# Kernel tuning notes

Hardware: AMD Instinct MI355X
Metric: run time of the kernel (lower is better)

## Reference

```python
import jax, jax.numpy as jnp
import numpy as np

NEG_SLOPE = 0.2  # PyG GATConv default leaky_relu slope


def gat_conv(x, src, dst, num_nodes, W, att_src, att_dst, bias, heads, out_ch, concat):
    """PyG-style GATConv (eval mode, self-loops already included in src/dst).
    x: [N, in_ch]; src/dst: [E] int; W: [in_ch, heads*out_ch];
    att_src/att_dst: [heads, out_ch]; bias: [heads*out_ch] or [out_ch].
    """
    N = num_nodes
    h = (x @ W).reshape(N, heads, out_ch)                      # [N, H, C]
    a_src = jnp.einsum('nhc,hc->nh', h, att_src)               # [N, H]
    a_dst = jnp.einsum('nhc,hc->nh', h, att_dst)               # [N, H]
    e = jax.nn.leaky_relu(a_src[src] + a_dst[dst], NEG_SLOPE)  # [E, H]
    # segment softmax over incoming edges of each dst node
    m = jax.ops.segment_max(e, dst, num_segments=N)            # [N, H]
    m = jnp.where(jnp.isfinite(m), m, 0.0)
    w = jnp.exp(e - m[dst])                                    # [E, H]
    denom = jax.ops.segment_sum(w, dst, num_segments=N)        # [N, H]
    alpha = w / denom[dst]                                     # [E, H]
    msg = alpha[:, :, None] * h[src]                           # [E, H, C]
    out = jax.ops.segment_sum(msg, dst, num_segments=N)        # [N, H, C]
    if concat:
        out = out.reshape(N, heads * out_ch)
    else:
        out = out.mean(axis=1)
    return out + bias


def setup_inputs() -> dict:
    key = jax.random.key(0)
    ks = jax.random.split(key, 10)
    N, E, in_ch, hidden, heads = 50000, 800000, 128, 64, 4
    x = jax.random.normal(ks[0], (N, in_ch), dtype=jnp.float32)
    edge_index = jax.random.randint(ks[1], (2, E), 0, N, dtype=jnp.int64)
    s1 = float(np.sqrt(1.0 / in_ch))
    W1 = jax.random.normal(ks[2], (in_ch, heads * hidden), dtype=jnp.float32) * s1
    att_src1 = jax.random.normal(ks[3], (heads, hidden), dtype=jnp.float32) * 0.1
    att_dst1 = jax.random.normal(ks[4], (heads, hidden), dtype=jnp.float32) * 0.1
    bias1 = jnp.zeros((heads * hidden,), dtype=jnp.float32)
    s2 = float(np.sqrt(1.0 / (heads * hidden)))
    W2 = jax.random.normal(ks[5], (heads * hidden, 1), dtype=jnp.float32) * s2
    att_src2 = jax.random.normal(ks[6], (1, 1), dtype=jnp.float32) * 0.1
    att_dst2 = jax.random.normal(ks[7], (1, 1), dtype=jnp.float32) * 0.1
    bias2 = jnp.zeros((1,), dtype=jnp.float32)
    return {"x": x, "edge_index": edge_index, "W1": W1, "att_src1": att_src1,
            "att_dst1": att_dst1, "bias1": bias1, "W2": W2, "att_src2": att_src2,
            "att_dst2": att_dst2, "bias2": bias2}


def reference(x, edge_index, W1, att_src1, att_dst1, bias1, W2, att_src2, att_dst2, bias2):
    N = x.shape[0]
    hidden, heads = 64, 4
    loops = jnp.arange(N, dtype=edge_index.dtype)
    src = jnp.concatenate([edge_index[0], loops])  # PyG adds self-loops
    dst = jnp.concatenate([edge_index[1], loops])
    # eval mode -> dropout is identity
    h = gat_conv(x, src, dst, N, W1, att_src1, att_dst1, bias1, heads, hidden, True)
    h = jax.nn.elu(h)
    out = gat_conv(h, src, dst, N, W2, att_src2, att_dst2, bias2, 1, 1, False)
    return out.squeeze(-1)  # [N]
```

## Files before the change

kernel.cpp:

```cpp
#include <hip/hip_runtime.h>
#include <hip/hip_fp16.h>
#include <math.h>

#define INC 128
#define F1 256
#define HEADS 4
#define NEG_SLOPE 0.2f

typedef _Float16 f16x8 __attribute__((ext_vector_type(8)));
typedef float f32x4 __attribute__((ext_vector_type(4)));

__global__ __launch_bounds__(256) void prep_kernel(
    const float* __restrict__ W1, _Float16* __restrict__ W1T,
    const int* __restrict__ ei, int* __restrict__ deg, int* __restrict__ rank,
    int E, int Etot, int nw1t)
{
    int b = blockIdx.x;
    if (b < nw1t) {
        int i = b * 256 + threadIdx.x;
        int k = i >> 8;
        int c = i & 255;
        W1T[c * 128 + k] = (_Float16)W1[i];
    } else {
        int e = (b - nw1t) * 256 + threadIdx.x;
        if (e < Etot) {
            int d = (e < E) ? ei[E + e] : (e - E);
            rank[e] = atomicAdd(&deg[d], 1);
        }
    }
}

__global__ __launch_bounds__(256) void scan1_kernel(
    const int* __restrict__ deg, int* __restrict__ incl,
    int* __restrict__ bsum, int N)
{
    __shared__ int tmp[256];
    int i = blockIdx.x * 256 + threadIdx.x;
    int v = (i < N) ? deg[i] : 0;
    tmp[threadIdx.x] = v;
    __syncthreads();
    for (int o = 1; o < 256; o <<= 1) {
        int add = (threadIdx.x >= o) ? tmp[threadIdx.x - o] : 0;
        __syncthreads();
        tmp[threadIdx.x] += add;
        __syncthreads();
    }
    if (i < N) incl[i] = tmp[threadIdx.x];
    if (threadIdx.x == 255) bsum[blockIdx.x] = tmp[255];
}

__global__ __launch_bounds__(256) void scan3_kernel(
    const int* __restrict__ deg, const int* __restrict__ incl,
    const int* __restrict__ bsum, int* __restrict__ off,
    int N, int Etot, int nb)
{
    __shared__ int tmp[256];
    const int bid = blockIdx.x;
    const int t = threadIdx.x;
    tmp[t] = (t < bid && t < nb) ? bsum[t] : 0;
    __syncthreads();
    #pragma unroll
    for (int o = 128; o > 0; o >>= 1) {
        if (t < o) tmp[t] += tmp[t + o];
        __syncthreads();
    }
    int pre = tmp[0];
    int i = bid * 256 + t;
    if (i < N) {
        off[i] = incl[i] - deg[i] + pre;
    } else if (i == N) {
        off[N] = Etot;
    }
}

__global__ __launch_bounds__(256, 4) void gemm_fill_kernel(
    const float* __restrict__ x, const _Float16* __restrict__ W1T,
    const float* __restrict__ att_s, const float* __restrict__ att_d,
    __half* __restrict__ h1, float* __restrict__ a_src, float* __restrict__ a_dst,
    const int* __restrict__ ei, const int* __restrict__ rank,
    const int* __restrict__ off, int* __restrict__ esrc,
    int N, int E, int Etot, int ngemm)
{
    __shared__ __align__(16) char smem[64 * 264 * 2];

    if ((int)blockIdx.x >= ngemm) {
        int e = (blockIdx.x - ngemm) * 256 + threadIdx.x;
        if (e < Etot) {
            int s, d;
            if (e < E) { s = ei[e]; d = ei[E + e]; }
            else       { s = d = e - E; }
            esrc[off[d] + rank[e]] = s;
        }
        return;
    }

    _Float16* xh = (_Float16*)smem;
    _Float16* ol = (_Float16*)smem;

    const int tid = threadIdx.x;
    const int wave = tid >> 6;
    const int lane = tid & 63;
    const int q = lane >> 4;
    const int c16 = lane & 15;
    const int row0 = blockIdx.x * 64;

    #pragma unroll
    for (int it = 0; it < 8; ++it) {
        int idx = (tid + it * 256) << 2;
        int r = idx >> 7;
        int c = idx & 127;
        int row = row0 + r;
        float4 v = (row < N) ? *(const float4*)&x[(size_t)row * INC + c]
                             : make_float4(0.f, 0.f, 0.f, 0.f);
        __half2 p0 = __floats2half2_rn(v.x, v.y);
        __half2 p1 = __floats2half2_rn(v.z, v.w);
        uint2 pk;
        pk.x = *(unsigned int*)&p0;
        pk.y = *(unsigned int*)&p1;
        *(uint2*)&xh[r * 136 + c] = pk;
    }
    __syncthreads();

    f16x8 afrag[4];
    #pragma unroll
    for (int kc = 0; kc < 4; ++kc)
        afrag[kc] = *(const f16x8*)&xh[(wave * 16 + c16) * 136 + kc * 32 + q * 8];
    __syncthreads();

    float psS[4][4] = {};
    float psD[4][4] = {};

    #pragma unroll
    for (int nc = 0; nc < 16; ++nc) {
        const int head = nc >> 2;
        const int col = nc * 16 + c16;
        f32x4 acc = {0.f, 0.f, 0.f, 0.f};
        f16x8 b0 = *(const f16x8*)&W1T[(size_t)col * 128 + 0 * 32 + q * 8];
        f16x8 b1 = *(const f16x8*)&W1T[(size_t)col * 128 + 1 * 32 + q * 8];
        f16x8 b2 = *(const f16x8*)&W1T[(size_t)col * 128 + 2 * 32 + q * 8];
        f16x8 b3 = *(const f16x8*)&W1T[(size_t)col * 128 + 3 * 32 + q * 8];
        acc = __builtin_amdgcn_mfma_f32_16x16x32_f16(afrag[0], b0, acc, 0, 0, 0);
        acc = __builtin_amdgcn_mfma_f32_16x16x32_f16(afrag[1], b1, acc, 0, 0, 0);
        acc = __builtin_amdgcn_mfma_f32_16x16x32_f16(afrag[2], b2, acc, 0, 0, 0);
        acc = __builtin_amdgcn_mfma_f32_16x16x32_f16(afrag[3], b3, acc, 0, 0, 0);

        float avs = att_s[col];
        float avd = att_d[col];
        #pragma unroll
        for (int reg = 0; reg < 4; ++reg) {
            float v = acc[reg];
            psS[reg][head] += v * avs;
            psD[reg][head] += v * avd;
            int row = wave * 16 + q * 4 + reg;
            ol[row * 264 + col] = (_Float16)v;
        }
    }

    #pragma unroll
    for (int o = 1; o < 16; o <<= 1) {
        #pragma unroll
        for (int reg = 0; reg < 4; ++reg)
            #pragma unroll
            for (int h = 0; h < 4; ++h) {
                psS[reg][h] += __shfl_xor(psS[reg][h], o);
                psD[reg][h] += __shfl_xor(psD[reg][h], o);
            }
    }
    if (c16 == 0) {
        #pragma unroll
        for (int reg = 0; reg < 4; ++reg) {
            int row = row0 + wave * 16 + q * 4 + reg;
            if (row < N) {
                float4 vs = make_float4(psS[reg][0], psS[reg][1], psS[reg][2], psS[reg][3]);
                float4 vd = make_float4(psD[reg][0], psD[reg][1], psD[reg][2], psD[reg][3]);
                *(float4*)&a_src[row * HEADS] = vs;
                *(float4*)&a_dst[row * HEADS] = vd;
            }
        }
    }

    __syncthreads();
    {
        int r = tid >> 2;
        int cq = (tid & 3) * 64;
        int row = row0 + r;
        if (row < N) {
            #pragma unroll
            for (int j = 0; j < 8; ++j) {
                uint4 v = *(uint4*)&ol[r * 264 + cq + j * 8];
                *(uint4*)&h1[(size_t)row * F1 + cq + j * 8] = v;
            }
        }
    }
}

__global__ __launch_bounds__(256) void agg1_kernel(
    const __half* __restrict__ h1, const float* __restrict__ a_src,
    const float* __restrict__ a_dst, const int* __restrict__ off,
    const int* __restrict__ esrc, const float* __restrict__ bias1,
    const float* __restrict__ W2, float* __restrict__ z, int N)
{
    __shared__ unsigned lalh[4][64][4];
    __shared__ int lsrc_s[4][64];

    const int wave = threadIdx.x >> 6;
    const int lane = threadIdx.x & 63;
    const int n = blockIdx.x * 4 + wave;
    if (n >= N) return;

    const int beg = off[n], end = off[n + 1];
    const int deg = end - beg;
    const float4* a_src4 = (const float4*)a_src;
    const uint2* h2 = (const uint2*)h1;
    float4 ad4 = *(const float4*)&a_dst[n * HEADS];
    float ad[4] = {ad4.x, ad4.y, ad4.z, ad4.w};
    const int head = lane >> 4;

    __half2 acc01 = __float2half2_rn(0.f);
    __half2 acc23 = __float2half2_rn(0.f);

    #define GATHER(CNT)                                                          \
    {                                                                            \
        int j = 0;                                                               \
        for (; j + 4 <= (CNT); j += 4) {                                         \
            int s0 = lsrc_s[wave][j + 0];                                        \
            int s1 = lsrc_s[wave][j + 1];                                        \
            int s2 = lsrc_s[wave][j + 2];                                        \
            int s3 = lsrc_s[wave][j + 3];                                        \
            uint2 v0 = h2[(size_t)s0 * 64 + lane];                               \
            uint2 v1 = h2[(size_t)s1 * 64 + lane];                               \
            uint2 v2 = h2[(size_t)s2 * 64 + lane];                               \
            uint2 v3 = h2[(size_t)s3 * 64 + lane];                               \
            unsigned a0 = lalh[wave][j + 0][head];                               \
            unsigned a1 = lalh[wave][j + 1][head];                               \
            unsigned a2 = lalh[wave][j + 2][head];                               \
            unsigned a3 = lalh[wave][j + 3][head];                               \
            acc01 = __hfma2(*(__half2*)&a0, *(__half2*)&v0.x, acc01);            \
            acc23 = __hfma2(*(__half2*)&a0, *(__half2*)&v0.y, acc23);            \
            acc01 = __hfma2(*(__half2*)&a1, *(__half2*)&v1.x, acc01);            \
            acc23 = __hfma2(*(__half2*)&a1, *(__half2*)&v1.y, acc23);            \
            acc01 = __hfma2(*(__half2*)&a2, *(__half2*)&v2.x, acc01);            \
            acc23 = __hfma2(*(__half2*)&a2, *(__half2*)&v2.y, acc23);            \
            acc01 = __hfma2(*(__half2*)&a3, *(__half2*)&v3.x, acc01);            \
            acc23 = __hfma2(*(__half2*)&a3, *(__half2*)&v3.y, acc23);            \
        }                                                                        \
        for (; j < (CNT); ++j) {                                                 \
            int s0 = lsrc_s[wave][j];                                            \
            unsigned a0 = lalh[wave][j][head];                                   \
            uint2 v0 = h2[(size_t)s0 * 64 + lane];                               \
            acc01 = __hfma2(*(__half2*)&a0, *(__half2*)&v0.x, acc01);            \
            acc23 = __hfma2(*(__half2*)&a0, *(__half2*)&v0.y, acc23);            \
        }                                                                        \
    }

    if (deg <= 64) {
        int i = beg + lane;
        bool valid = i < end;
        int sN = esrc[valid ? i : beg];
        float4 a4 = a_src4[sN];
        float av[4] = {a4.x, a4.y, a4.z, a4.w};
        float ev[4];
        #pragma unroll
        for (int h = 0; h < 4; ++h) {
            float e = av[h] + ad[h];
            e = e > 0.f ? e : NEG_SLOPE * e;
            ev[h] = valid ? e : -1e30f;
        }
        float m[4] = {ev[0], ev[1], ev[2], ev[3]};
        #pragma unroll
        for (int o = 32; o > 0; o >>= 1) {
            #pragma unroll
            for (int h = 0; h < 4; ++h) m[h] = fmaxf(m[h], __shfl_xor(m[h], o));
        }
        float at[4];
        #pragma unroll
        for (int h = 0; h < 4; ++h) at[h] = valid ? __expf(ev[h] - m[h]) : 0.f;
        float s[4] = {at[0], at[1], at[2], at[3]};
        #pragma unroll
        for (int o = 32; o > 0; o >>= 1) {
            #pragma unroll
            for (int h = 0; h < 4; ++h) s[h] += __shfl_xor(s[h], o);
        }
        #pragma unroll
        for (int h = 0; h < 4; ++h) {
            __half2 a2h = __float2half2_rn(at[h] / s[h]);
            lalh[wave][lane][h] = *(unsigned*)&a2h;
        }
        lsrc_s[wave][lane] = sN;

        GATHER(deg);
    } else {
        float m[4] = {-1e30f, -1e30f, -1e30f, -1e30f};
        float s[4] = {0.f, 0.f, 0.f, 0.f};
        for (int i = beg + lane; i < end; i += 64) {
            int sN = esrc[i];
            float4 a4 = a_src4[sN];
            float av[4] = {a4.x, a4.y, a4.z, a4.w};
            #pragma unroll
            for (int h = 0; h < 4; ++h) {
                float e = av[h] + ad[h];
                e = e > 0.f ? e : NEG_SLOPE * e;
                float nm = fmaxf(m[h], e);
                s[h] = s[h] * __expf(m[h] - nm) + __expf(e - nm);
                m[h] = nm;
            }
        }
        #pragma unroll
        for (int o = 32; o > 0; o >>= 1) {
            #pragma unroll
            for (int h = 0; h < 4; ++h) {
                float om = __shfl_xor(m[h], o);
                float os = __shfl_xor(s[h], o);
                float nm = fmaxf(m[h], om);
                s[h] = s[h] * __expf(m[h] - nm) + os * __expf(om - nm);
                m[h] = nm;
            }
        }
        float inv[4];
        #pragma unroll
        for (int h = 0; h < 4; ++h) inv[h] = 1.f / s[h];

        for (int c0 = beg; c0 < end; c0 += 64) {
            int i = c0 + lane;
            if (i < end) {
                int sN = esrc[i];
                float4 a4 = a_src4[sN];
                float av[4] = {a4.x, a4.y, a4.z, a4.w};
                #pragma unroll
                for (int h = 0; h < 4; ++h) {
                    float e = av[h] + ad[h];
                    e = e > 0.f ? e : NEG_SLOPE * e;
                    __half2 a2h = __float2half2_rn(__expf(e - m[h]) * inv[h]);
                    lalh[wave][lane][h] = *(unsigned*)&a2h;
                }
                lsrc_s[wave][lane] = sN;
            }
            int cend = end - c0;
            if (cend > 64) cend = 64;
            GATHER(cend);
        }
    }
    #undef GATHER

    float acc0 = __half2float(acc01.x);
    float acc1 = __half2float(acc01.y);
    float acc2 = __half2float(acc23.x);
    float acc3 = __half2float(acc23.y);
    float4 b4 = *(const float4*)&bias1[lane << 2];
    float4 w24 = *(const float4*)&W2[lane << 2];
    float o0 = acc0 + b4.x, o1 = acc1 + b4.y, o2 = acc2 + b4.z, o3 = acc3 + b4.w;
    o0 = o0 > 0.f ? o0 : __expf(o0) - 1.f;
    o1 = o1 > 0.f ? o1 : __expf(o1) - 1.f;
    o2 = o2 > 0.f ? o2 : __expf(o2) - 1.f;
    o3 = o3 > 0.f ? o3 : __expf(o3) - 1.f;
    float p = o0 * w24.x + o1 * w24.y + o2 * w24.z + o3 * w24.w;
    #pragma unroll
    for (int o = 32; o > 0; o >>= 1) p += __shfl_xor(p, o);
    if (lane == 0) z[n] = p;
}

__global__ __launch_bounds__(256) void agg2_kernel(
    const float* __restrict__ z, const int* __restrict__ off,
    const int* __restrict__ esrc, const float* __restrict__ att_s2,
    const float* __restrict__ att_d2, const float* __restrict__ bias2,
    float* __restrict__ out, int N)
{
    int wave = threadIdx.x >> 6;
    int lane = threadIdx.x & 63;
    int n = blockIdx.x * 4 + wave;
    if (n >= N) return;
    float as2 = att_s2[0], ad2 = att_d2[0];
    int beg = off[n], end = off[n + 1];
    int deg = end - beg;
    float dstterm = z[n] * ad2;

    if (deg <= 64) {
        int i = beg + lane;
        bool valid = i < end;
        int sN = esrc[valid ? i : beg];
        float zv = z[sN];
        float e = zv * as2 + dstterm;
        e = e > 0.f ? e : NEG_SLOPE * e;
        float ev = valid ? e : -1e30f;
        float m = ev;
        #pragma unroll
        for (int o = 32; o > 0; o >>= 1) m = fmaxf(m, __shfl_xor(m, o));
        float at = valid ? __expf(ev - m) : 0.f;
        float s = at, w = at * zv;
        #pragma unroll
        for (int o = 32; o > 0; o >>= 1) {
            s += __shfl_xor(s, o);
            w += __shfl_xor(w, o);
        }
        if (lane == 0) out[n] = w / s + bias2[0];
    } else {
        float m = -1e30f, s = 0.f, w = 0.f;
        for (int i = beg + lane; i < end; i += 64) {
            int sN = esrc[i];
            float zv = z[sN];
            float e = zv * as2 + dstterm;
            e = e > 0.f ? e : NEG_SLOPE * e;
            float nm = fmaxf(m, e);
            float c0 = __expf(m - nm), c1 = __expf(e - nm);
            s = s * c0 + c1;
            w = w * c0 + c1 * zv;
            m = nm;
        }
        #pragma unroll
        for (int o = 32; o > 0; o >>= 1) {
            float om = __shfl_xor(m, o), os = __shfl_xor(s, o), ow = __shfl_xor(w, o);
            float nm = fmaxf(m, om);
            float c0 = __expf(m - nm), c1 = __expf(om - nm);
            s = s * c0 + os * c1;
            w = w * c0 + ow * c1;
            m = nm;
        }
        if (lane == 0) out[n] = w / s + bias2[0];
    }
}

extern "C" void kernel_launch(void* const* d_in, const int* in_sizes, int n_in,
                              void* d_out, int out_size, void* d_ws, size_t ws_size,
                              hipStream_t stream)
{
    const float* x        = (const float*)d_in[0];
    const int*   ei       = (const int*)d_in[1];
    const float* W1       = (const float*)d_in[2];
    const float* att_src1 = (const float*)d_in[3];
    const float* att_dst1 = (const float*)d_in[4];
    const float* bias1    = (const float*)d_in[5];
    const float* W2       = (const float*)d_in[6];
    const float* att_src2 = (const float*)d_in[7];
    const float* att_dst2 = (const float*)d_in[8];
    const float* bias2    = (const float*)d_in[9];
    float* out = (float*)d_out;

    int N = in_sizes[0] / INC;
    int E = in_sizes[1] / 2;
    int Etot = E + N;

    char* p = (char*)d_ws;
    auto alloc = [&](size_t bytes) {
        void* r = (void*)p;
        p += (bytes + 255) & ~(size_t)255;
        return r;
    };
    __half* h1      = (__half*)alloc((size_t)N * F1 * 2);
    _Float16* W1T   = (_Float16*)alloc((size_t)INC * F1 * 2);
    float* a_src1 = (float*)alloc((size_t)N * HEADS * 4);
    float* a_dst1 = (float*)alloc((size_t)N * HEADS * 4);
    float* z      = (float*)alloc((size_t)N * 4);
    int* deg    = (int*)alloc((size_t)N * 4);
    int* incl   = (int*)alloc((size_t)N * 4);
    int* off    = (int*)alloc((size_t)(N + 1) * 4);
    int* rank   = (int*)alloc((size_t)Etot * 4);
    int* bsum   = (int*)alloc(1024);
    int* esrc   = (int*)alloc((size_t)Etot * 4);

    hipMemsetAsync(deg, 0, (size_t)N * 4, stream);

    int nw1t = INC * F1 / 256;
    int egrid = (Etot + 255) / 256;
    prep_kernel<<<nw1t + egrid, 256, 0, stream>>>(W1, W1T, ei, deg, rank, E, Etot, nw1t);

    int nb = (N + 255) / 256;
    scan1_kernel<<<nb, 256, 0, stream>>>(deg, incl, bsum, N);

    int nb1 = (N + 1 + 255) / 256;
    scan3_kernel<<<nb1, 256, 0, stream>>>(deg, incl, bsum, off, N, Etot, nb);

    int ngemm = (N + 63) / 64;
    gemm_fill_kernel<<<ngemm + egrid, 256, 0, stream>>>(
        x, W1T, att_src1, att_dst1, h1, a_src1, a_dst1,
        ei, rank, off, esrc, N, E, Etot, ngemm);

    int ngrid1 = (N + 3) / 4;
    agg1_kernel<<<ngrid1, 256, 0, stream>>>(h1, a_src1, a_dst1, off, esrc, bias1, W2, z, N);

    int ngrid2 = (N + 3) / 4;
    agg2_kernel<<<ngrid2, 256, 0, stream>>>(z, off, esrc, att_src2, att_dst2, bias2, out, N);
}
```

Measured before the change: 175.0 us.

## Aggregate raw fp16 inputs per head before the layer-1 GEMM

Uses linearity to reorder layer 1. It first aggregates attention-weighted fp16 input features (128 channels, four heads) per destination node, then applies W1 per head with MFMA in a new gemm2 kernel fused with bias, ELU and the W2 projection. Attention logits come from x through precomputed folded vectors W1·att, built in prep_kernel. The gathered row per edge shrinks from 256 to 128 halves, at the cost of a written and re-read 512-wide per-node aggregate buffer and a different fp16 rounding order.

```diff
diff --git a/kernel.cpp b/kernel.cpp
--- a/kernel.cpp
+++ b/kernel.cpp
@@ -12,6 +12,8 @@
 
 __global__ __launch_bounds__(256) void prep_kernel(
     const float* __restrict__ W1, _Float16* __restrict__ W1T,
+    const float* __restrict__ att_s, const float* __restrict__ att_d,
+    float* __restrict__ w1s, float* __restrict__ w1d,
     const int* __restrict__ ei, int* __restrict__ deg, int* __restrict__ rank,
     int E, int Etot, int nw1t)
 {
@@ -21,11 +23,26 @@
         int k = i >> 8;
         int c = i & 255;
         W1T[c * 128 + k] = (_Float16)W1[i];
-    } else {
+    } else if (b < nw1t + ((Etot + 255) >> 8)) {
         int e = (b - nw1t) * 256 + threadIdx.x;
         if (e < Etot) {
             int d = (e < E) ? ei[E + e] : (e - E);
             rank[e] = atomicAdd(&deg[d], 1);
+        }
+    } else {
+        #pragma unroll
+        for (int rep = 0; rep < 2; ++rep) {
+            int idx = threadIdx.x + rep * 256;
+            int h = idx >> 7;
+            int k = idx & 127;
+            float ss = 0.f, sd = 0.f;
+            for (int c = 0; c < 64; ++c) {
+                float w = W1[k * F1 + h * 64 + c];
+                ss += w * att_s[h * 64 + c];
+                sd += w * att_d[h * 64 + c];
+            }
+            w1s[h * 128 + k] = ss;
+            w1d[h * 128 + k] = sd;
         }
     }
 }
@@ -73,18 +90,16 @@
     }
 }
 
-__global__ __launch_bounds__(256, 4) void gemm_fill_kernel(
-    const float* __restrict__ x, const _Float16* __restrict__ W1T,
-    const float* __restrict__ att_s, const float* __restrict__ att_d,
-    __half* __restrict__ h1, float* __restrict__ a_src, float* __restrict__ a_dst,
+__global__ __launch_bounds__(256) void mid_kernel(
     const int* __restrict__ ei, const int* __restrict__ rank,
     const int* __restrict__ off, int* __restrict__ esrc,
-    int N, int E, int Etot, int ngemm)
-{
-    __shared__ __align__(16) char smem[64 * 264 * 2];
-
-    if ((int)blockIdx.x >= ngemm) {
-        int e = (blockIdx.x - ngemm) * 256 + threadIdx.x;
+    const float* __restrict__ x, const float* __restrict__ w1s,
+    const float* __restrict__ w1d, float* __restrict__ a_src,
+    float* __restrict__ a_dst, unsigned* __restrict__ x_h,
+    int N, int E, int Etot, int egrid)
+{
+    if ((int)blockIdx.x < egrid) {
+        int e = blockIdx.x * 256 + threadIdx.x;
         if (e < Etot) {
             int s, d;
             if (e < E) { s = ei[e]; d = ei[E + e]; }
@@ -93,112 +108,39 @@
         }
         return;
     }
-
-    _Float16* xh = (_Float16*)smem;
-    _Float16* ol = (_Float16*)smem;
-
-    const int tid = threadIdx.x;
-    const int wave = tid >> 6;
-    const int lane = tid & 63;
-    const int q = lane >> 4;
-    const int c16 = lane & 15;
-    const int row0 = blockIdx.x * 64;
-
-    #pragma unroll
-    for (int it = 0; it < 8; ++it) {
-        int idx = (tid + it * 256) << 2;
-        int r = idx >> 7;
-        int c = idx & 127;
-        int row = row0 + r;
-        float4 v = (row < N) ? *(const float4*)&x[(size_t)row * INC + c]
-                             : make_float4(0.f, 0.f, 0.f, 0.f);
-        __half2 p0 = __floats2half2_rn(v.x, v.y);
-        __half2 p1 = __floats2half2_rn(v.z, v.w);
-        uint2 pk;
-        pk.x = *(unsigned int*)&p0;
-        pk.y = *(unsigned int*)&p1;
-        *(uint2*)&xh[r * 136 + c] = pk;
-    }
-    __syncthreads();
-
-    f16x8 afrag[4];
-    #pragma unroll
-    for (int kc = 0; kc < 4; ++kc)
-        afrag[kc] = *(const f16x8*)&xh[(wave * 16 + c16) * 136 + kc * 32 + q * 8];
-    __syncthreads();
-
-    float psS[4][4] = {};
-    float psD[4][4] = {};
-
-    #pragma unroll
-    for (int nc = 0; nc < 16; ++nc) {
-        const int head = nc >> 2;
-        const int col = nc * 16 + c16;
-        f32x4 acc = {0.f, 0.f, 0.f, 0.f};
-        f16x8 b0 = *(const f16x8*)&W1T[(size_t)col * 128 + 0 * 32 + q * 8];
-        f16x8 b1 = *(const f16x8*)&W1T[(size_t)col * 128 + 1 * 32 + q * 8];
-        f16x8 b2 = *(const f16x8*)&W1T[(size_t)col * 128 + 2 * 32 + q * 8];
-        f16x8 b3 = *(const f16x8*)&W1T[(size_t)col * 128 + 3 * 32 + q * 8];
-        acc = __builtin_amdgcn_mfma_f32_16x16x32_f16(afrag[0], b0, acc, 0, 0, 0);
-        acc = __builtin_amdgcn_mfma_f32_16x16x32_f16(afrag[1], b1, acc, 0, 0, 0);
-        acc = __builtin_amdgcn_mfma_f32_16x16x32_f16(afrag[2], b2, acc, 0, 0, 0);
-        acc = __builtin_amdgcn_mfma_f32_16x16x32_f16(afrag[3], b3, acc, 0, 0, 0);
-
-        float avs = att_s[col];
-        float avd = att_d[col];
-        #pragma unroll
-        for (int reg = 0; reg < 4; ++reg) {
-            float v = acc[reg];
-            psS[reg][head] += v * avs;
-            psD[reg][head] += v * avd;
-            int row = wave * 16 + q * 4 + reg;
-            ol[row * 264 + col] = (_Float16)v;
-        }
-    }
-
-    #pragma unroll
-    for (int o = 1; o < 16; o <<= 1) {
-        #pragma unroll
-        for (int reg = 0; reg < 4; ++reg)
-            #pragma unroll
-            for (int h = 0; h < 4; ++h) {
-                psS[reg][h] += __shfl_xor(psS[reg][h], o);
-                psD[reg][h] += __shfl_xor(psD[reg][h], o);
-            }
-    }
-    if (c16 == 0) {
-        #pragma unroll
-        for (int reg = 0; reg < 4; ++reg) {
-            int row = row0 + wave * 16 + q * 4 + reg;
-            if (row < N) {
-                float4 vs = make_float4(psS[reg][0], psS[reg][1], psS[reg][2], psS[reg][3]);
-                float4 vd = make_float4(psD[reg][0], psD[reg][1], psD[reg][2], psD[reg][3]);
-                *(float4*)&a_src[row * HEADS] = vs;
-                *(float4*)&a_dst[row * HEADS] = vd;
-            }
-        }
-    }
-
-    __syncthreads();
-    {
-        int r = tid >> 2;
-        int cq = (tid & 3) * 64;
-        int row = row0 + r;
-        if (row < N) {
-            #pragma unroll
-            for (int j = 0; j < 8; ++j) {
-                uint4 v = *(uint4*)&ol[r * 264 + cq + j * 8];
-                *(uint4*)&h1[(size_t)row * F1 + cq + j * 8] = v;
-            }
-        }
-    }
-}
-
-__global__ __launch_bounds__(256) void agg1_kernel(
-    const __half* __restrict__ h1, const float* __restrict__ a_src,
+    int wave = threadIdx.x >> 6;
+    int lane = threadIdx.x & 63;
+    int n = (blockIdx.x - egrid) * 4 + wave;
+    if (n >= N) return;
+    float2 xv = *(const float2*)&x[(size_t)n * INC + lane * 2];
+    __half2 xh = __floats2half2_rn(xv.x, xv.y);
+    x_h[(size_t)n * 64 + lane] = *(unsigned*)&xh;
+    float ps[4], pd[4];
+    #pragma unroll
+    for (int h = 0; h < 4; ++h) {
+        float2 ws = *(const float2*)&w1s[h * 128 + lane * 2];
+        float2 wd = *(const float2*)&w1d[h * 128 + lane * 2];
+        ps[h] = xv.x * ws.x + xv.y * ws.y;
+        pd[h] = xv.x * wd.x + xv.y * wd.y;
+    }
+    #pragma unroll
+    for (int o = 32; o > 0; o >>= 1) {
+        #pragma unroll
+        for (int h = 0; h < 4; ++h) {
+            ps[h] += __shfl_xor(ps[h], o);
+            pd[h] += __shfl_xor(pd[h], o);
+        }
+    }
+    if (lane == 0) {
+        *(float4*)&a_src[n * HEADS] = make_float4(ps[0], ps[1], ps[2], ps[3]);
+        *(float4*)&a_dst[n * HEADS] = make_float4(pd[0], pd[1], pd[2], pd[3]);
+    }
+}
+
+__global__ __launch_bounds__(256) void aggx_kernel(
+    const unsigned* __restrict__ x_h, const float* __restrict__ a_src,
     const float* __restrict__ a_dst, const int* __restrict__ off,
-    const int* __restrict__ esrc, const float* __restrict__ bias1,
-    const float* __restrict__ W2, float* __restrict__ z, int N)
+    const int* __restrict__ esrc, __half* __restrict__ agg, int N)
 {
     __shared__ unsigned lalh[4][64][4];
     __shared__ int lsrc_s[4][64];
@@ -211,13 +153,12 @@
     const int beg = off[n], end = off[n + 1];
     const int deg = end - beg;
     const float4* a_src4 = (const float4*)a_src;
-    const uint2* h2 = (const uint2*)h1;
     float4 ad4 = *(const float4*)&a_dst[n * HEADS];
     float ad[4] = {ad4.x, ad4.y, ad4.z, ad4.w};
-    const int head = lane >> 4;
-
-    __half2 acc01 = __float2half2_rn(0.f);
-    __half2 acc23 = __float2half2_rn(0.f);
+
+    __half2 acc[4];
+    #pragma unroll
+    for (int h = 0; h < 4; ++h) acc[h] = __float2half2_rn(0.f);
 
     #define GATHER(CNT)                                                          \
     {                                                                            \
@@ -227,29 +168,42 @@
             int s1 = lsrc_s[wave][j + 1];                                        \
             int s2 = lsrc_s[wave][j + 2];                                        \
             int s3 = lsrc_s[wave][j + 3];                                        \
-            uint2 v0 = h2[(size_t)s0 * 64 + lane];                               \
-            uint2 v1 = h2[(size_t)s1 * 64 + lane];                               \
-            uint2 v2 = h2[(size_t)s2 * 64 + lane];                               \
-            uint2 v3 = h2[(size_t)s3 * 64 + lane];                               \
-            unsigned a0 = lalh[wave][j + 0][head];                               \
-            unsigned a1 = lalh[wave][j + 1][head];                               \
-            unsigned a2 = lalh[wave][j + 2][head];                               \
-            unsigned a3 = lalh[wave][j + 3][head];                               \
-            acc01 = __hfma2(*(__half2*)&a0, *(__half2*)&v0.x, acc01);            \
-            acc23 = __hfma2(*(__half2*)&a0, *(__half2*)&v0.y, acc23);            \
-            acc01 = __hfma2(*(__half2*)&a1, *(__half2*)&v1.x, acc01);            \
-            acc23 = __hfma2(*(__half2*)&a1, *(__half2*)&v1.y, acc23);            \
-            acc01 = __hfma2(*(__half2*)&a2, *(__half2*)&v2.x, acc01);            \
-            acc23 = __hfma2(*(__half2*)&a2, *(__half2*)&v2.y, acc23);            \
-            acc01 = __hfma2(*(__half2*)&a3, *(__half2*)&v3.x, acc01);            \
-            acc23 = __hfma2(*(__half2*)&a3, *(__half2*)&v3.y, acc23);            \
+            unsigned v0 = x_h[(size_t)s0 * 64 + lane];                           \
+            unsigned v1 = x_h[(size_t)s1 * 64 + lane];                           \
+            unsigned v2 = x_h[(size_t)s2 * 64 + lane];                           \
+            unsigned v3 = x_h[(size_t)s3 * 64 + lane];                           \
+            uint4 a0 = *(uint4*)&lalh[wave][j + 0][0];                           \
+            uint4 a1 = *(uint4*)&lalh[wave][j + 1][0];                           \
+            uint4 a2 = *(uint4*)&lalh[wave][j + 2][0];                           \
+            uint4 a3 = *(uint4*)&lalh[wave][j + 3][0];                           \
+            __half2 h0 = *(__half2*)&v0, h1v = *(__half2*)&v1;                   \
+            __half2 h2v = *(__half2*)&v2, h3 = *(__half2*)&v3;                   \
+            acc[0] = __hfma2(*(__half2*)&a0.x, h0, acc[0]);                      \
+            acc[1] = __hfma2(*(__half2*)&a0.y, h0, acc[1]);                      \
+            acc[2] = __hfma2(*(__half2*)&a0.z, h0, acc[2]);                      \
+            acc[3] = __hfma2(*(__half2*)&a0.w, h0, acc[3]);                      \
+            acc[0] = __hfma2(*(__half2*)&a1.x, h1v, acc[0]);                     \
+            acc[1] = __hfma2(*(__half2*)&a1.y, h1v, acc[1]);                     \
+            acc[2] = __hfma2(*(__half2*)&a1.z, h1v, acc[2]);                     \
+            acc[3] = __hfma2(*(__half2*)&a1.w, h1v, acc[3]);                     \
+            acc[0] = __hfma2(*(__half2*)&a2.x, h2v, acc[0]);                     \
+            acc[1] = __hfma2(*(__half2*)&a2.y, h2v, acc[1]);                     \
+            acc[2] = __hfma2(*(__half2*)&a2.z, h2v, acc[2]);                     \
+            acc[3] = __hfma2(*(__half2*)&a2.w, h2v, acc[3]);                     \
+            acc[0] = __hfma2(*(__half2*)&a3.x, h3, acc[0]);                      \
+            acc[1] = __hfma2(*(__half2*)&a3.y, h3, acc[1]);                      \
+            acc[2] = __hfma2(*(__half2*)&a3.z, h3, acc[2]);                      \
+            acc[3] = __hfma2(*(__half2*)&a3.w, h3, acc[3]);                      \
         }                                                                        \
         for (; j < (CNT); ++j) {                                                 \
             int s0 = lsrc_s[wave][j];                                            \
-            unsigned a0 = lalh[wave][j][head];                                   \
-            uint2 v0 = h2[(size_t)s0 * 64 + lane];                               \
-            acc01 = __hfma2(*(__half2*)&a0, *(__half2*)&v0.x, acc01);            \
-            acc23 = __hfma2(*(__half2*)&a0, *(__half2*)&v0.y, acc23);            \
+            unsigned v0 = x_h[(size_t)s0 * 64 + lane];                           \
+            uint4 a0 = *(uint4*)&lalh[wave][j][0];                               \
+            __half2 h0 = *(__half2*)&v0;                                         \
+            acc[0] = __hfma2(*(__half2*)&a0.x, h0, acc[0]);                      \
+            acc[1] = __hfma2(*(__half2*)&a0.y, h0, acc[1]);                      \
+            acc[2] = __hfma2(*(__half2*)&a0.z, h0, acc[2]);                      \
+            acc[3] = __hfma2(*(__half2*)&a0.w, h0, acc[3]);                      \
         }                                                                        \
     }
 
@@ -281,11 +235,14 @@
             #pragma unroll
             for (int h = 0; h < 4; ++h) s[h] += __shfl_xor(s[h], o);
         }
-        #pragma unroll
-        for (int h = 0; h < 4; ++h) {
-            __half2 a2h = __float2half2_rn(at[h] / s[h]);
-            lalh[wave][lane][h] = *(unsigned*)&a2h;
-        }
+        uint4 pack;
+        __half2 t0 = __float2half2_rn(at[0] / s[0]);
+        __half2 t1 = __float2half2_rn(at[1] / s[1]);
+        __half2 t2 = __float2half2_rn(at[2] / s[2]);
+        __half2 t3 = __float2half2_rn(at[3] / s[3]);
+        pack.x = *(unsigned*)&t0; pack.y = *(unsigned*)&t1;
+        pack.z = *(unsigned*)&t2; pack.w = *(unsigned*)&t3;
+        *(uint4*)&lalh[wave][lane][0] = pack;
         lsrc_s[wave][lane] = sN;
 
         GATHER(deg);
@@ -326,13 +283,15 @@
                 int sN = esrc[i];
                 float4 a4 = a_src4[sN];
                 float av[4] = {a4.x, a4.y, a4.z, a4.w};
+                uint4 pack;
                 #pragma unroll
                 for (int h = 0; h < 4; ++h) {
                     float e = av[h] + ad[h];
                     e = e > 0.f ? e : NEG_SLOPE * e;
                     __half2 a2h = __float2half2_rn(__expf(e - m[h]) * inv[h]);
-                    lalh[wave][lane][h] = *(unsigned*)&a2h;
+                    ((unsigned*)&pack)[h] = *(unsigned*)&a2h;
                 }
+                *(uint4*)&lalh[wave][lane][0] = pack;
                 lsrc_s[wave][lane] = sN;
             }
             int cend = end - c0;
@@ -342,21 +301,88 @@
     }
     #undef GATHER
 
-    float acc0 = __half2float(acc01.x);
-    float acc1 = __half2float(acc01.y);
-    float acc2 = __half2float(acc23.x);
-    float acc3 = __half2float(acc23.y);
-    float4 b4 = *(const float4*)&bias1[lane << 2];
-    float4 w24 = *(const float4*)&W2[lane << 2];
-    float o0 = acc0 + b4.x, o1 = acc1 + b4.y, o2 = acc2 + b4.z, o3 = acc3 + b4.w;
-    o0 = o0 > 0.f ? o0 : __expf(o0) - 1.f;
-    o1 = o1 > 0.f ? o1 : __expf(o1) - 1.f;
-    o2 = o2 > 0.f ? o2 : __expf(o2) - 1.f;
-    o3 = o3 > 0.f ? o3 : __expf(o3) - 1.f;
-    float p = o0 * w24.x + o1 * w24.y + o2 * w24.z + o3 * w24.w;
-    #pragma unroll
-    for (int o = 32; o > 0; o >>= 1) p += __shfl_xor(p, o);
-    if (lane == 0) z[n] = p;
+    #pragma unroll
+    for (int h = 0; h < 4; ++h)
+        *(unsigned*)&agg[(size_t)n * 512 + h * 128 + lane * 2] = *(unsigned*)&acc[h];
+}
+
+__global__ __launch_bounds__(256, 4) void gemm2_kernel(
+    const __half* __restrict__ agg, const _Float16* __restrict__ W1T,
+    const float* __restrict__ bias1, const float* __restrict__ W2,
+    float* __restrict__ z, int N)
+{
+    __shared__ __align__(16) _Float16 stg[32 * 520];
+    __shared__ float zpart[2][32];
+
+    const int tid = threadIdx.x;
+    const int w = tid >> 6;
+    const int lane = tid & 63;
+    const int q = lane >> 4;
+    const int c16 = lane & 15;
+    const int row0 = blockIdx.x * 32;
+    const int rg = w & 1;
+    const int cg = w >> 1;
+
+    #pragma unroll
+    for (int it = 0; it < 8; ++it) {
+        int flat = (tid + it * 256) * 8;
+        int r = flat >> 9;
+        int c = flat & 511;
+        int row = row0 + r;
+        uint4 v = (row < N) ? *(const uint4*)&agg[(size_t)row * 512 + c]
+                            : make_uint4(0, 0, 0, 0);
+        *(uint4*)&stg[r * 520 + c] = v;
+    }
+    __syncthreads();
+
+    const int row_l = rg * 16 + c16;
+    f16x8 af[2][4];
+    #pragma unroll
+    for (int hh = 0; hh < 2; ++hh) {
+        int h = cg * 2 + hh;
+        #pragma unroll
+        for (int kc = 0; kc < 4; ++kc)
+            af[hh][kc] = *(const f16x8*)&stg[row_l * 520 + h * 128 + kc * 32 + q * 8];
+    }
+
+    float pz[4] = {};
+    #pragma unroll
+    for (int hh = 0; hh < 2; ++hh) {
+        #pragma unroll
+        for (int t = 0; t < 4; ++t) {
+            int col = cg * 128 + hh * 64 + t * 16 + c16;
+            f32x4 acc = {0.f, 0.f, 0.f, 0.f};
+            #pragma unroll
+            for (int kc = 0; kc < 4; ++kc) {
+                f16x8 b = *(const f16x8*)&W1T[(size_t)col * 128 + kc * 32 + q * 8];
+                acc = __builtin_amdgcn_mfma_f32_16x16x32_f16(af[hh][kc], b, acc, 0, 0, 0);
+            }
+            float bv = bias1[col];
+            float wv = W2[col];
+            #pragma unroll
+            for (int reg = 0; reg < 4; ++reg) {
+                float o = acc[reg] + bv;
+                o = o > 0.f ? o : __expf(o) - 1.f;
+                pz[reg] = fmaf(o, wv, pz[reg]);
+            }
+        }
+    }
+
+    #pragma unroll
+    for (int o = 8; o > 0; o >>= 1) {
+        #pragma unroll
+        for (int reg = 0; reg < 4; ++reg) pz[reg] += __shfl_xor(pz[reg], o);
+    }
+    if (c16 == 0) {
+        #pragma unroll
+        for (int reg = 0; reg < 4; ++reg)
+            zpart[cg][rg * 16 + q * 4 + reg] = pz[reg];
+    }
+    __syncthreads();
+    if (tid < 32) {
+        int row = row0 + tid;
+        if (row < N) z[row] = zpart[0][tid] + zpart[1][tid];
+    }
 }
 
 __global__ __launch_bounds__(256) void agg2_kernel(
@@ -386,15 +412,15 @@
         #pragma unroll
         for (int o = 32; o > 0; o >>= 1) m = fmaxf(m, __shfl_xor(m, o));
         float at = valid ? __expf(ev - m) : 0.f;
-        float s = at, w = at * zv;
+        float s = at, wv = at * zv;
         #pragma unroll
         for (int o = 32; o > 0; o >>= 1) {
             s += __shfl_xor(s, o);
-            w += __shfl_xor(w, o);
-        }
-        if (lane == 0) out[n] = w / s + bias2[0];
+            wv += __shfl_xor(wv, o);
+        }
+        if (lane == 0) out[n] = wv / s + bias2[0];
     } else {
-        float m = -1e30f, s = 0.f, w = 0.f;
+        float m = -1e30f, s = 0.f, wv = 0.f;
         for (int i = beg + lane; i < end; i += 64) {
             int sN = esrc[i];
             float zv = z[sN];
@@ -403,19 +429,19 @@
             float nm = fmaxf(m, e);
             float c0 = __expf(m - nm), c1 = __expf(e - nm);
             s = s * c0 + c1;
-            w = w * c0 + c1 * zv;
+            wv = wv * c0 + c1 * zv;
             m = nm;
         }
         #pragma unroll
         for (int o = 32; o > 0; o >>= 1) {
-            float om = __shfl_xor(m, o), os = __shfl_xor(s, o), ow = __shfl_xor(w, o);
+            float om = __shfl_xor(m, o), os = __shfl_xor(s, o), ow = __shfl_xor(wv, o);
             float nm = fmaxf(m, om);
             float c0 = __expf(m - nm), c1 = __expf(om - nm);
             s = s * c0 + os * c1;
-            w = w * c0 + ow * c1;
+            wv = wv * c0 + ow * c1;
             m = nm;
         }
-        if (lane == 0) out[n] = w / s + bias2[0];
+        if (lane == 0) out[n] = wv / s + bias2[0];
     }
 }
 
@@ -445,8 +471,11 @@
         p += (bytes + 255) & ~(size_t)255;
         return r;
     };
-    __half* h1      = (__half*)alloc((size_t)N * F1 * 2);
+    unsigned* x_h   = (unsigned*)alloc((size_t)N * 64 * 4);
+    __half* agg     = (__half*)alloc((size_t)N * 512 * 2);
     _Float16* W1T   = (_Float16*)alloc((size_t)INC * F1 * 2);
+    float* w1s    = (float*)alloc(4 * 128 * 4);
+    float* w1d    = (float*)alloc(4 * 128 * 4);
     float* a_src1 = (float*)alloc((size_t)N * HEADS * 4);
     float* a_dst1 = (float*)alloc((size_t)N * HEADS * 4);
     float* z      = (float*)alloc((size_t)N * 4);
@@ -461,7 +490,8 @@
 
     int nw1t = INC * F1 / 256;
     int egrid = (Etot + 255) / 256;
-    prep_kernel<<<nw1t + egrid, 256, 0, stream>>>(W1, W1T, ei, deg, rank, E, Etot, nw1t);
+    prep_kernel<<<nw1t + egrid + 1, 256, 0, stream>>>(
+        W1, W1T, att_src1, att_dst1, w1s, w1d, ei, deg, rank, E, Etot, nw1t);
 
     int nb = (N + 255) / 256;
     scan1_kernel<<<nb, 256, 0, stream>>>(deg, incl, bsum, N);
@@ -469,13 +499,15 @@
     int nb1 = (N + 1 + 255) / 256;
     scan3_kernel<<<nb1, 256, 0, stream>>>(deg, incl, bsum, off, N, Etot, nb);
 
-    int ngemm = (N + 63) / 64;
-    gemm_fill_kernel<<<ngemm + egrid, 256, 0, stream>>>(
-        x, W1T, att_src1, att_dst1, h1, a_src1, a_dst1,
-        ei, rank, off, esrc, N, E, Etot, ngemm);
+    int nlog = (N + 3) / 4;
+    mid_kernel<<<egrid + nlog, 256, 0, stream>>>(
+        ei, rank, off, esrc, x, w1s, w1d, a_src1, a_dst1, x_h, N, E, Etot, egrid);
 
     int ngrid1 = (N + 3) / 4;
-    agg1_kernel<<<ngrid1, 256, 0, stream>>>(h1, a_src1, a_dst1, off, esrc, bias1, W2, z, N);
+    aggx_kernel<<<ngrid1, 256, 0, stream>>>(x_h, a_src1, a_dst1, off, esrc, agg, N);
+
+    int ng2 = (N + 31) / 32;
+    gemm2_kernel<<<ng2, 256, 0, stream>>>(agg, W1T, bias1, W2, z, N);
 
     int ngrid2 = (N + 3) / 4;
     agg2_kernel<<<ngrid2, 256, 0, stream>>>(z, off, esrc, att_src2, att_dst2, bias2, out, N);
```

Result: slower. 181.5 us (+3.7%).
